# Kernel tuning notes

Hardware: AMD Instinct MI355X
Metric: run time of the kernel (lower is better)

The kernel has to match this reference:

```python
import jax, jax.numpy as jnp
import numpy as np

B, L, D, H = 2, 4096, 1024, 4
DV = D // H
NP = 5
MIN_PROB = 0.01
CHUNK = 32
RIN = D + H * NP * 4 + H * (NP * (NP - 1)) // 2  # 1144
RH = 2 * RIN


def dwconv_causal(x, w):
    # x: (B, L, C); w: (C, K) depthwise causal FIR
    K = w.shape[-1]
    xp = jnp.pad(x, ((0, 0), (K - 1, 0), (0, 0))).transpose(0, 2, 1)  # (B,C,L+K-1)
    y = jax.lax.conv_general_dilated(
        xp, w[:, None, :], window_strides=(1,), padding='VALID',
        feature_group_count=w.shape[0],
        dimension_numbers=('NCH', 'OIH', 'NCH'))
    return y.transpose(0, 2, 1)  # (B,L,C)


def l2norm(x):
    return x * jax.lax.rsqrt(jnp.sum(x * x, -1, keepdims=True) + 1e-12)


def delta_rule_chunkwise(q, k, v, beta, chunk=CHUNK):
    # q,k: (b,h,L,dk)  v: (b,h,L,dv)  beta: (b,h,L); L divisible by chunk
    b, h, Lq, dk = q.shape
    dv = v.shape[-1]
    n = Lq // chunk
    q = l2norm(q); k = l2norm(k)
    v = v * beta[..., None]
    kb = k * beta[..., None]
    r = lambda x: x.reshape(b, h, n, chunk, -1)
    q, k, v, kb = r(q), r(k), r(v), r(kb)
    tri = jnp.triu(jnp.ones((chunk, chunk), bool), 0)
    attn = jnp.where(tri, 0.0, -(kb @ jnp.swapaxes(k, -1, -2)))
    for i in range(1, chunk):  # in-chunk triangular-inverse recurrence
        upd = jnp.einsum('...k,...ki->...i', attn[..., i, :], attn[..., :, :i])
        attn = attn.at[..., i, :i].add(upd)
    attn = attn + jnp.eye(chunk, dtype=attn.dtype)
    u = attn @ v
    w = attn @ kb
    strict = jnp.triu(jnp.ones((chunk, chunk), bool), 1)

    def step(S, inp):
        qi, ki, ui, wi = inp
        la = jnp.where(strict, 0.0, qi @ jnp.swapaxes(ki, -1, -2))
        u_i = ui - wi @ S
        o_i = qi @ S + la @ u_i
        return S + jnp.swapaxes(ki, -1, -2) @ u_i, o_i

    mv = lambda x: jnp.moveaxis(x, 2, 0)
    S0 = jnp.zeros((b, h, dk, dv), q.dtype)
    S, o = jax.lax.scan(step, S0, (mv(q), mv(k), mv(u), mv(w)))
    return jnp.moveaxis(o, 0, 2).reshape(b, h, Lq, dv), S


def setup_inputs() -> dict:
    key = jax.random.key(0)
    ks = jax.random.split(key, 20)
    f = lambda k, shape, s=0.02: jax.random.normal(k, shape, jnp.float32) * s
    # FIR filters: identity tap (last) + small noise, matching learned-from-delta init
    def fir(k, ksz):
        w = np.zeros((D, ksz), np.float32)
        w[:, -1] = 1.0
        return jnp.asarray(w) + f(k, (D, ksz), 0.02)
    b2 = np.zeros((H, NP), np.float32)
    b2[:, -1] = 0.5
    b2[:, -2] = 0.5
    return {
        'hidden_states': jax.random.normal(ks[0], (B, L, D), jnp.float32),
        'Wq': f(ks[1], (D, D)), 'Wk': f(ks[2], (D, D)), 'Wv': f(ks[3], (D, D)),
        'wq_conv': f(ks[4], (D, 4), 0.2), 'wk_conv': f(ks[5], (D, 4), 0.2),
        'wv_conv': f(ks[6], (D, 4), 0.2),
        'Wb': f(ks[7], (H, D)),
        'fir_s_w': fir(ks[8], 3), 'fir_m_w': fir(ks[9], 7),
        'fir_l_w': fir(ks[10], 25), 'fir_id_w': fir(ks[11], 1),
        'W1': f(ks[12], (RH, RIN)), 'b1': jnp.zeros((RH,), jnp.float32),
        'W2': f(ks[13], (H * NP, RH)), 'b2': jnp.asarray(b2.reshape(-1)),
        'norm_w': jnp.ones((DV,), jnp.float32),
        'Wo': f(ks[14], (D, D)),
    }


def reference(hidden_states, Wq, Wk, Wv, wq_conv, wk_conv, wv_conv, Wb,
              fir_s_w, fir_m_w, fir_l_w, fir_id_w, W1, b1, W2, b2, norm_w, Wo):
    silu = jax.nn.silu
    q = silu(dwconv_causal(hidden_states @ Wq.T, wq_conv))
    k = silu(dwconv_causal(hidden_states @ Wk.T, wk_conv))
    v = silu(dwconv_causal(hidden_states @ Wv.T, wv_conv))
    beta = jax.nn.sigmoid(hidden_states @ Wb.T)  # (B,L,H)
    q4 = q.reshape(B, L, H, -1).transpose(0, 2, 1, 3)
    k4 = k.reshape(B, L, H, -1).transpose(0, 2, 1, 3)
    v4 = v.reshape(B, L, H, -1).transpose(0, 2, 1, 3)
    delta_out, _ = delta_rule_chunkwise(q4, k4, v4, beta.transpose(0, 2, 1))
    delta_out = delta_out.transpose(0, 2, 1, 3)  # (B,L,H,DV)
    fir = lambda w: dwconv_causal(v, w).reshape(B, L, H, DV)
    branches = [fir(fir_s_w), fir(fir_m_w), fir(fir_l_w), delta_out, fir(fir_id_w)]
    feats = []
    for x in branches:
        sm = jax.nn.softmax(x, -1)
        feats += [x.mean(-1), jnp.var(x, -1, ddof=1), jnp.max(x, -1),
                  -(sm * jnp.log(sm + 1e-8)).sum(-1)]
    cross = []
    for i in range(NP):
        for j in range(i + 1, NP):
            xi, xj = branches[i], branches[j]
            den = jnp.sqrt(jnp.sum(xi * xi, -1)) * jnp.sqrt(jnp.sum(xj * xj, -1)) + 1e-8
            cross.append(jnp.sum(xi * xj, -1) / den)
    router_in = jnp.concatenate([hidden_states] + feats + cross, axis=-1)  # (B,L,RIN)
    hrt = jax.nn.gelu(router_in @ W1.T + b1, approximate=False)
    logits = (hrt @ W2.T + b2).reshape(B, L, H, NP)
    p = jax.nn.softmax(logits, -1)
    p = p * (1.0 - NP * MIN_PROB) + MIN_PROB  # probability floor
    out = jnp.einsum('blhp,pblhd->blhd', p, jnp.stack(branches))
    out = out * jax.lax.rsqrt(jnp.mean(out * out, -1, keepdims=True) + 1e-5) * norm_w
    return out.reshape(B, L, H * DV) @ Wo.T
```

## Files before the change

### kernel.cpp

```cpp
#include <hip/hip_runtime.h>
#include <stdint.h>

typedef unsigned short u16t;
typedef u16t us4 __attribute__((ext_vector_type(4)));
typedef u16t us8 __attribute__((ext_vector_type(8)));
typedef __bf16 bf8v __attribute__((ext_vector_type(8)));
typedef float f4 __attribute__((ext_vector_type(4)));

#define MFMA(a, b, c) __builtin_amdgcn_mfma_f32_16x16x32_bf16((a), (b), (c), 0, 0, 0)
#define GLOAD_LDS16(g, l) __builtin_amdgcn_global_load_lds( \
    (const __attribute__((address_space(1))) void*)(g),     \
    (__attribute__((address_space(3))) void*)(l), 16, 0, 0)

__device__ __forceinline__ float bf2f(u16t u) {
  union { unsigned int i; float f; } c; c.i = ((unsigned int)u) << 16; return c.f;
}
__device__ __forceinline__ u16t f2bf(float f) {
  union { float f; unsigned int i; } c; c.f = f;
  return (u16t)((c.i + 0x7FFFu + ((c.i >> 16) & 1u)) >> 16);
}
__device__ __forceinline__ float wsum(float v) {
#pragma unroll
  for (int o = 32; o > 0; o >>= 1) v += __shfl_xor(v, o);
  return v;
}
__device__ __forceinline__ float wmax(float v) {
#pragma unroll
  for (int o = 32; o > 0; o >>= 1) v = fmaxf(v, __shfl_xor(v, o));
  return v;
}

__global__ __launch_bounds__(256) void pack_all(const float* __restrict__ hid,
    const float* __restrict__ Wq, const float* __restrict__ Wk, const float* __restrict__ Wv,
    u16t* __restrict__ hidb, u16t* __restrict__ wqb, u16t* __restrict__ wkb,
    u16t* __restrict__ wvb) {
  const int g = blockIdx.x * 256 + threadIdx.x;
  const float* src; u16t* dst; int off;
  if (g < 2097152) { src = hid; dst = hidb; off = g; }
  else if (g < 2359296) { src = Wq; dst = wqb; off = g - 2097152; }
  else if (g < 2621440) { src = Wk; dst = wkb; off = g - 2359296; }
  else { src = Wv; dst = wvb; off = g - 2621440; }
  f4 v = *(const f4*)&src[(size_t)off * 4];
  us4 o;
#pragma unroll
  for (int e = 0; e < 4; ++e) o[e] = f2bf(v[e]);
  *(us4*)&dst[(size_t)off * 4] = o;
}

__global__ __launch_bounds__(256) void pack_bf16(const float* __restrict__ src,
    u16t* __restrict__ dst, int n4) {
  const int i = blockIdx.x * 256 + threadIdx.x;
  if (i >= n4) return;
  f4 v = *(const f4*)&src[(size_t)i * 4];
  us4 o;
#pragma unroll
  for (int e = 0; e < 4; ++e) o[e] = f2bf(v[e]);
  *(us4*)&dst[(size_t)i * 4] = o;
}

template <bool CF32, int EPI>
__device__ __forceinline__ void gemm_body(const u16t* __restrict__ A,
    const u16t* __restrict__ Bt, void* __restrict__ Cv, const float* __restrict__ bias,
    int K, int lda, int ldb, int ldc, int m0, int n0) {
  __shared__ u16t As[128][32];
  __shared__ u16t Bs[128][32];
  const int tid = threadIdx.x;
  const int wv = tid >> 6, l = tid & 63;
  const int wr = wv >> 1, wc = wv & 1;
  const int lr = l & 15, kg8 = (l >> 4) * 8, rg4 = (l >> 4) * 4;
  const f4 zf = {0.f, 0.f, 0.f, 0.f};
  f4 acc[4][4];
#pragma unroll
  for (int i = 0; i < 4; ++i)
#pragma unroll
    for (int j = 0; j < 4; ++j) acc[i][j] = zf;

  const u16t* ga = A + (size_t)(m0 + wv * 32 + (l >> 2)) * lda + (l & 3) * 8;
  const u16t* gb = Bt + (size_t)(n0 + wv * 32 + (l >> 2)) * ldb + (l & 3) * 8;
  u16t* la0 = &As[wv * 32][0];
  u16t* la1 = &As[wv * 32 + 16][0];
  u16t* lb0 = &Bs[wv * 32][0];
  u16t* lb1 = &Bs[wv * 32 + 16][0];

  for (int kt = 0; kt < K; kt += 32) {
    GLOAD_LDS16(ga + kt, la0);
    GLOAD_LDS16(ga + (size_t)16 * lda + kt, la1);
    GLOAD_LDS16(gb + kt, lb0);
    GLOAD_LDS16(gb + (size_t)16 * ldb + kt, lb1);
    __syncthreads();
    bf8v af[4], bg[4];
#pragma unroll
    for (int f = 0; f < 4; ++f) af[f] = *(const bf8v*)&As[wr * 64 + f * 16 + lr][kg8];
#pragma unroll
    for (int f = 0; f < 4; ++f) bg[f] = *(const bf8v*)&Bs[wc * 64 + f * 16 + lr][kg8];
#pragma unroll
    for (int i = 0; i < 4; ++i)
#pragma unroll
      for (int j = 0; j < 4; ++j) acc[i][j] = MFMA(af[i], bg[j], acc[i][j]);
    __syncthreads();
  }
#pragma unroll
  for (int i = 0; i < 4; ++i) {
    const int rb = m0 + wr * 64 + i * 16 + rg4;
#pragma unroll
    for (int j = 0; j < 4; ++j) {
      const int cb = n0 + wc * 64 + j * 16 + lr;
#pragma unroll
      for (int r = 0; r < 4; ++r) {
        float x = acc[i][j][r];
        if (EPI == 1) {
          float xx = x + ((cb < 2288) ? bias[cb] : 0.f);
          x = 0.5f * xx * (1.f + erff(xx * 0.70710678118f));
        }
        if (CF32)
          ((float*)Cv)[(size_t)(rb + r) * ldc + cb] = x;
        else
          ((u16t*)Cv)[(size_t)(rb + r) * ldc + cb] = f2bf(x);
      }
    }
  }
}

template <bool CF32, int EPI>
__global__ __launch_bounds__(256) void gemm_bt(const u16t* __restrict__ Av,
    const u16t* __restrict__ Btv, void* __restrict__ Cv, const float* __restrict__ bias,
    int K, int lda, int ldb, int ldc) {
  gemm_body<CF32, EPI>(Av, Btv, Cv, bias, K, lda, ldb, ldc,
                       blockIdx.y * 128, blockIdx.x * 128);
}

__global__ __launch_bounds__(256) void gemm_qkv3(const u16t* __restrict__ A,
    const u16t* __restrict__ B0, const u16t* __restrict__ B1,
    const u16t* __restrict__ B2, u16t* __restrict__ C0, u16t* __restrict__ C1,
    u16t* __restrict__ C2v) {
  const int z = blockIdx.z;
  const u16t* Bt = (z == 0) ? B0 : ((z == 1) ? B1 : B2);
  u16t* C = (z == 0) ? C0 : ((z == 1) ? C1 : C2v);
  gemm_body<false, 0>(A, Bt, C, nullptr, 1024, 1024, 1024, 1024,
                      blockIdx.y * 128, blockIdx.x * 128);
}
// ... 14 lines not shown
  for (int i = 0; i < 67; ++i) {
    int ls = l0 - 3 + i;
    sm[i][tid] = (ls >= 0) ? in_[((size_t)b * 4096 + ls) * 1024 + c] : (u16t)0;
  }
  __syncthreads();
  f4 w4 = *(const f4*)&w_[c * 4];
  float x0 = bf2f(sm[0][tid]), x1 = bf2f(sm[1][tid]), x2 = bf2f(sm[2][tid]);
  for (int ll = 0; ll < 64; ++ll) {
    float x3 = bf2f(sm[ll + 3][tid]);
    float y = x0 * w4[0] + x1 * w4[1] + x2 * w4[2] + x3 * w4[3];
    y = y / (1.f + expf(-y));
    out_[((size_t)b * 4096 + l0 + ll) * 1024 + c] = f2bf(y);
    x0 = x1; x1 = x2; x2 = x3;
  }
}

__global__ __launch_bounds__(256) void prep_kernel(u16t* __restrict__ qc, u16t* __restrict__ kc,
    const u16t* __restrict__ vc, const float* __restrict__ hid, const float* __restrict__ Wb,
    u16t* __restrict__ kbeta, u16t* __restrict__ vbeta) {
  const int m = blockIdx.x, tid = threadIdx.x;
  const int h = tid >> 6, l = tid & 63;
  float bacc = 0.f;
#pragma unroll
  for (int it = 0; it < 4; ++it) {
    int kk = l * 4 + it * 256;
    f4 hv = *(const f4*)&hid[(size_t)m * 1024 + kk];
    f4 wv4 = *(const f4*)&Wb[(size_t)h * 1024 + kk];
#pragma unroll
    for (int e = 0; e < 4; ++e) bacc += hv[e] * wv4[e];
  }
  const float bet = 1.f / (1.f + expf(-wsum(bacc)));
  const size_t base = (size_t)m * 1024 + h * 256 + l * 4;
  us4 q4 = *(const us4*)&qc[base];
  float qf[4]; float ss = 0.f;
#pragma unroll
  for (int e = 0; e < 4; ++e) { qf[e] = bf2f(q4[e]); ss += qf[e] * qf[e]; }
  float qsc = rsqrtf(wsum(ss) + 1e-12f);
  us4 qo;
#pragma unroll
  for (int e = 0; e < 4; ++e) qo[e] = f2bf(qf[e] * qsc);
  *(us4*)&qc[base] = qo;
  us4 k4 = *(const us4*)&kc[base];
  float kf[4]; ss = 0.f;
#pragma unroll
  for (int e = 0; e < 4; ++e) { kf[e] = bf2f(k4[e]); ss += kf[e] * kf[e]; }
  float ksc = rsqrtf(wsum(ss) + 1e-12f);
  us4 ko, kbo;
#pragma unroll
  for (int e = 0; e < 4; ++e) {
    float kn = kf[e] * ksc;
    ko[e] = f2bf(kn);
    kbo[e] = f2bf(kn * bet);
  }
  *(us4*)&kc[base] = ko;
  *(us4*)&kbeta[base] = kbo;
  us4 v4 = *(const us4*)&vc[base];
  us4 vo;
#pragma unroll
  for (int e = 0; e < 4; ++e) vo[e] = f2bf(bf2f(v4[e]) * bet);
  *(us4*)&vbeta[base] = vo;
}

__global__ __launch_bounds__(256) void chunk_uw(const u16t* __restrict__ kn,
    const u16t* __restrict__ kbeta, const u16t* __restrict__ vbeta,
    u16t* __restrict__ ug, u16t* __restrict__ wg) {
  const int tid = threadIdx.x;
  const int bh = blockIdx.x >> 7, ci = blockIdx.x & 127;
  const int b = bh >> 2, h = bh & 3;
  const int l0 = ci * 32;
  __shared__ u16t kns[32][264], kbs[32][264], vbs[32][264];
  __shared__ float attn_s[32][33];
  const int sr = tid >> 5, sd8 = (tid & 31) * 8;
  const size_t rowbase = (size_t)b * 4096 * 1024 + (size_t)h * 256;
#pragma unroll
  for (int i = 0; i < 4; ++i) {
    int r = i * 8 + sr;
    size_t g = rowbase + (size_t)(l0 + r) * 1024 + sd8;
    *(us8*)&kns[r][sd8] = *(const us8*)&kn[g];
    *(us8*)&kbs[r][sd8] = *(const us8*)&kbeta[g];
    *(us8*)&vbs[r][sd8] = *(const us8*)&vbeta[g];
  }
  __syncthreads();
  {
    const int i = tid >> 3, j4 = (tid & 7) * 4;
    float d0 = 0.f, d1 = 0.f, d2 = 0.f, d3 = 0.f;
    for (int d8 = 0; d8 < 256; d8 += 8) {
      us8 kb8 = *(const us8*)&kbs[i][d8];
      us8 n0v = *(const us8*)&kns[j4][d8];
      us8 n1v = *(const us8*)&kns[j4 + 1][d8];
      us8 n2v = *(const us8*)&kns[j4 + 2][d8];
      us8 n3v = *(const us8*)&kns[j4 + 3][d8];
#pragma unroll
      for (int e = 0; e < 8; ++e) {
        float kv = bf2f(kb8[e]);
        d0 += kv * bf2f(n0v[e]); d1 += kv * bf2f(n1v[e]);
        d2 += kv * bf2f(n2v[e]); d3 += kv * bf2f(n3v[e]);
      }
    }
    attn_s[i][j4]     = (j4     < i) ? -d0 : 0.f;
    attn_s[i][j4 + 1] = (j4 + 1 < i) ? -d1 : 0.f;
    attn_s[i][j4 + 2] = (j4 + 2 < i) ? -d2 : 0.f;
    attn_s[i][j4 + 3] = (j4 + 3 < i) ? -d3 : 0.f;
  }
  __syncthreads();
  if (tid < 32) {
    const int j = tid;
    for (int i = 1; i < 32; ++i) {
      float aij = attn_s[i][j];
      float upd = 0.f;
#pragma unroll 1
      for (int k = 1; k < 31; ++k) {
        float aik = __shfl(aij, k);
        float akj = (k > j && k < i) ? attn_s[k][j] : 0.f;
        upd += aik * akj;
      }
      if (j < i) attn_s[i][j] = aij + upd;
    }
    attn_s[j][j] = 1.f;
  }
  __syncthreads();
  {
    const int r = tid >> 3, cg = (tid & 7) * 32;
    float ua[32], wa[32];
#pragma unroll
    for (int e = 0; e < 32; ++e) { ua[e] = 0.f; wa[e] = 0.f; }
    for (int j = 0; j < 32; ++j) {
      float a = attn_s[r][j];
#pragma unroll
      for (int e0 = 0; e0 < 32; e0 += 8) {
        us8 v8 = *(const us8*)&vbs[j][cg + e0];
        us8 k8 = *(const us8*)&kbs[j][cg + e0];
#pragma unroll
        for (int e = 0; e < 8; ++e) {
          ua[e0 + e] += a * bf2f(v8[e]);
          wa[e0 + e] += a * bf2f(k8[e]);
        }
      }
    }
    const size_t ob = ((size_t)bh * 4096 + l0 + r) * 256 + cg;
#pragma unroll
    for (int e0 = 0; e0 < 32; e0 += 8) {
      us8 pu, pw;
#pragma unroll
      for (int e = 0; e < 8; ++e) { pu[e] = f2bf(ua[e0 + e]); pw[e] = f2bf(wa[e0 + e]); }
      *(us8*)&ug[ob + e0] = pu;
      *(us8*)&wg[ob + e0] = pw;
    }
  }
}

__global__ __launch_bounds__(256, 1) void delta_scan(const u16t* __restrict__ qn,
    const u16t* __restrict__ kn, const u16t* __restrict__ ug, const u16t* __restrict__ wg,
    u16t* __restrict__ dout, const u16t* __restrict__ vc, const float* __restrict__ w25g,
    u16t* __restrict__ fl, const float* __restrict__ W1, u16t* __restrict__ W1p,
    const float* __restrict__ Wo, u16t* __restrict__ wob) {
  const int blk = blockIdx.x;
  const int tid = threadIdx.x;
  if (blk < 32) {
    const int bh = blk >> 2, vbidx = blk & 3;
    const int b = bh >> 2, h = bh & 3;
    const int c0 = vbidx * 64;
    const int wv = tid >> 6, l = tid & 63;
    const int lr = l & 15, kg8 = (l >> 4) * 8, rg4 = (l >> 4) * 4;

    __shared__ u16t qs[32][264], ks2[32][264], wss[32][264];
    __shared__ u16t kts[256][40];
    __shared__ u16t sbf[64][264];
    __shared__ u16t las[32][40];
    __shared__ u16t uts[64][40];

    {
      u16t* sp = &sbf[0][0];
      for (int i = tid; i < 64 * 264; i += 256) sp[i] = 0;
    }
    const f4 zf = {0.f, 0.f, 0.f, 0.f};
    f4 sacc[16];
#pragma unroll
    for (int d = 0; d < 16; ++d) sacc[d] = zf;
    __syncthreads();

    const u16t* qb = qn + (size_t)b * 4096 * 1024 + (size_t)h * 256;
    const u16t* knb = kn + (size_t)b * 4096 * 1024 + (size_t)h * 256;
    const u16t* ub = ug + (size_t)bh * 4096 * 256;
    const u16t* wb = wg + (size_t)bh * 4096 * 256;
    const int sr = tid >> 5, sd8 = (tid & 31) * 8;

    us8 pq[4], pk[4], pw[4];
    us4 pu0, pu1;
#pragma unroll
    for (int i = 0; i < 4; ++i) {
      const int r = i * 8 + sr;
      pq[i] = *(const us8*)(qb + (size_t)r * 1024 + sd8);
      pk[i] = *(const us8*)(knb + (size_t)r * 1024 + sd8);
      pw[i] = *(const us8*)(wb + (size_t)r * 256 + sd8);
    }
    pu0 = *(const us4*)(ub + (size_t)lr * 256 + c0 + wv * 16 + rg4);
    pu1 = *(const us4*)(ub + (size_t)(16 + lr) * 256 + c0 + wv * 16 + rg4);

    for (int ci = 0; ci < 128; ++ci) {
      const int l0 = ci * 32;
#pragma unroll
      for (int i = 0; i < 4; ++i) {
        const int r = i * 8 + sr;
        *(us8*)&qs[r][sd8] = pq[i];
        *(us8*)&ks2[r][sd8] = pk[i];
        *(us8*)&wss[r][sd8] = pw[i];
      }
      const us4 u0 = pu0, u1 = pu1;
      __syncthreads();
      if (ci < 127) {
        const int l1 = l0 + 32;
#pragma unroll
        for (int i = 0; i < 4; ++i) {
          const int r = i * 8 + sr;
          pq[i] = *(const us8*)(qb + (size_t)(l1 + r) * 1024 + sd8);
          pk[i] = *(const us8*)(knb + (size_t)(l1 + r) * 1024 + sd8);
          pw[i] = *(const us8*)(wb + (size_t)(l1 + r) * 256 + sd8);
        }
        pu0 = *(const us4*)(ub + (size_t)(l1 + lr) * 256 + c0 + wv * 16 + rg4);
        pu1 = *(const us4*)(ub + (size_t)(l1 + 16 + lr) * 256 + c0 + wv * 16 + rg4);
      }
      {
        const int dk = tid;
        const int swz = ((dk >> 3) & 3) << 3;
#pragma unroll
        for (int r = 0; r < 32; r += 2) {
          unsigned int lo = ks2[r][dk], hi = ks2[r + 1][dk];
          *(unsigned int*)&kts[dk][r ^ swz] = lo | (hi << 16);
        }
      }
      {
        const int rq = wv >> 1, rk = wv & 1;
        f4 t4 = zf;
#pragma unroll
        for (int ks = 0; ks < 8; ++ks) {
          bf8v a = *(const bf8v*)&qs[rq * 16 + lr][ks * 32 + kg8];
          bf8v bb = *(const bf8v*)&ks2[rk * 16 + lr][ks * 32 + kg8];
          t4 = MFMA(a, bb, t4);
// ... 24 lines not shown
        for (int rt = 0; rt < 2; ++rt) {
          f4 mm = rt ? m1 : m0;
          const us4 uu = rt ? u1 : u0;
          const int r = rt * 16 + lr;
#pragma unroll
          for (int rr = 0; rr < 4; ++rr)
            uts[wv * 16 + rg4 + rr][r] = f2bf(bf2f(uu[rr]) - mm[rr]);
        }
      }
      __syncthreads();
      {
        bf8v a2 = *(const bf8v*)&uts[wv * 16 + lr][kg8];
        {
          bf8v lb0 = *(const bf8v*)&las[lr][kg8];
          bf8v lb1 = *(const bf8v*)&las[16 + lr][kg8];
          o0 = MFMA(a2, lb0, o0);
          o1 = MFMA(a2, lb1, o1);
        }
#pragma unroll
        for (int rt = 0; rt < 2; ++rt) {
          f4 oo = rt ? o1 : o0;
          const int r = rt * 16 + lr;
          us4 st;
#pragma unroll
          for (int rr = 0; rr < 4; ++rr) st[rr] = f2bf(oo[rr]);
          *(us4*)(dout + ((size_t)(b * 4096 + l0 + r) * 4 + h) * 256 + c0 + wv * 16 + rg4) = st;
        }
#pragma unroll
        for (int d = 0; d < 16; ++d) {
          const int swzd = ((2 * d + (lr >> 3)) & 3) << 3;
          bf8v bb = *(const bf8v*)&kts[d * 16 + lr][kg8 ^ swzd];
          sacc[d] = MFMA(a2, bb, sacc[d]);
        }
#pragma unroll
        for (int d = 0; d < 16; ++d) {
#pragma unroll
          for (int rr = 0; rr < 4; ++rr)
            sbf[wv * 16 + rg4 + rr][d * 16 + lr] = f2bf(sacc[d][rr]);
        }
      }
      __syncthreads();
    }
    return;
  }
  if (blk < 544) {
    const int fb = blk - 32;
    const int l0 = (fb & 63) * 64;
    const int by = fb >> 6;
    const int b = by >> 2, cb = by & 3;
    const int c = cb * 256 + tid;
    __shared__ u16t sm[88][256];
    for (int i = 0; i < 88; ++i) {
      int ls = l0 - 24 + i;
      sm[i][tid] = (ls >= 0) ? vc[((size_t)b * 4096 + ls) * 1024 + c] : (u16t)0;
    }
    __syncthreads();
    float w25[25];
#pragma unroll
    for (int j = 0; j < 25; ++j) w25[j] = w25g[c * 25 + j];
    float x[25];
#pragma unroll
    for (int j = 0; j < 25; ++j) x[j] = bf2f(sm[j][tid]);
    for (int ll = 0; ll < 64; ++ll) {
      float yl = 0.f;
#pragma unroll
      for (int j = 0; j < 25; ++j) yl += x[j] * w25[j];
      fl[((size_t)b * 4096 + l0 + ll) * 1024 + c] = f2bf(yl);
      if (ll < 63) {
#pragma unroll
        for (int j = 0; j < 24; ++j) x[j] = x[j + 1];
        x[24] = bf2f(sm[ll + 25][tid]);
      }
    }
    return;
  }
  if (blk < 672) {
    for (size_t idx = (size_t)(blk - 544) * 256 + tid; idx < (size_t)2304 * 1152;
         idx += (size_t)128 * 256) {
      int n = (int)(idx / 1152), k = (int)(idx % 1152);
      W1p[idx] = (n < 2288 && k < 1144) ? f2bf(W1[(size_t)n * 1144 + k]) : (u16t)0;
    }
    return;
  }
  for (size_t i = (size_t)(blk - 672) * 256 + tid; i < 262144; i += (size_t)64 * 256) {
    f4 v = *(const f4*)&Wo[i * 4];
    us4 o;
#pragma unroll
    for (int e = 0; e < 4; ++e) o[e] = f2bf(v[e]);
    *(us4*)&wob[i * 4] = o;
  }
}

__device__ __forceinline__ void fir_otf(const u16t* __restrict__ vc,
    const float* __restrict__ w3g, const float* __restrict__ w7g,
    const float* __restrict__ w1g, int b, int lseq, int c0,
    float ys[4], float ym[4], float yi[4]) {
  float xs[7][4];
#pragma unroll
  for (int j = 0; j < 7; ++j) {
    int ls = lseq - 6 + j;
    if (ls >= 0) {
      us4 v = *(const us4*)&vc[((size_t)b * 4096 + ls) * 1024 + c0];
#pragma unroll
      for (int e = 0; e < 4; ++e) xs[j][e] = bf2f(v[e]);
    } else {
#pragma unroll
      for (int e = 0; e < 4; ++e) xs[j][e] = 0.f;
    }
  }
#pragma unroll
  for (int e = 0; e < 4; ++e) {
    const int c = c0 + e;
    ys[e] = xs[4][e] * w3g[c * 3] + xs[5][e] * w3g[c * 3 + 1] + xs[6][e] * w3g[c * 3 + 2];
    float m_ = 0.f;
#pragma unroll
    for (int j = 0; j < 7; ++j) m_ += xs[j][e] * w7g[c * 7 + j];
    ym[e] = m_;
    yi[e] = xs[6][e] * w1g[c];
  }
}

__global__ __launch_bounds__(256) void features_kernel(const float* __restrict__ hid,
    const u16t* __restrict__ vc, const float* __restrict__ w3g, const float* __restrict__ w7g,
    const float* __restrict__ w1g, const u16t* __restrict__ fl, const u16t* __restrict__ dlt,
    u16t* __restrict__ router) {
  const int m = blockIdx.x, tid = threadIdx.x;
  const int h = tid >> 6, l = tid & 63;
  const int b = m >> 12, lseq = m & 4095;
  const int c0 = h * 256 + l * 4;
  const size_t base = (size_t)m * 1024 + c0;
  float x[5][4];
  fir_otf(vc, w3g, w7g, w1g, b, lseq, c0, x[0], x[1], x[4]);
  {
    us4 v2 = *(const us4*)&fl[base];
    us4 v3 = *(const us4*)&dlt[base];
#pragma unroll
    for (int e = 0; e < 4; ++e) { x[2][e] = bf2f(v2[e]); x[3][e] = bf2f(v3[e]); }
  }
  float s1[5], s2[5], mx[5];
#pragma unroll
  for (int br = 0; br < 5; ++br) {
    float a = 0.f, bq = 0.f, m_ = -1e30f;
#pragma unroll
    for (int e = 0; e < 4; ++e) {
      a += x[br][e]; bq += x[br][e] * x[br][e]; m_ = fmaxf(m_, x[br][e]);
    }
    s1[br] = wsum(a); s2[br] = wsum(bq); mx[br] = wmax(m_);
  }
  float ent[5];
#pragma unroll
  for (int br = 0; br < 5; ++br) {
    float e_ = 0.f;
#pragma unroll
    for (int e = 0; e < 4; ++e) e_ += expf(x[br][e] - mx[br]);
    float es = wsum(e_);
    float hn = 0.f;
#pragma unroll
    for (int e = 0; e < 4; ++e) {
      float pv = expf(x[br][e] - mx[br]) / es;
      hn += pv * logf(pv + 1e-8f);
    }
    ent[br] = -wsum(hn);
  }
  float dt[10];
  {
    int pi = 0;
#pragma unroll
    for (int i = 0; i < 5; ++i)
#pragma unroll
      for (int j = i + 1; j < 5; ++j) {
        float d = 0.f;
#pragma unroll
        for (int e = 0; e < 4; ++e) d += x[i][e] * x[j][e];
        dt[pi] = wsum(d);
        ++pi;
      }
  }
  if (l == 0) {
    u16t* rp = router + (size_t)m * 1152 + 1024;
#pragma unroll
    for (int br = 0; br < 5; ++br) {
      float mean = s1[br] * (1.f / 256.f);
      float var = (s2[br] - s1[br] * s1[br] * (1.f / 256.f)) * (1.f / 255.f);
      rp[br * 16 + 0 + h] = f2bf(mean);
      rp[br * 16 + 4 + h] = f2bf(var);
      rp[br * 16 + 8 + h] = f2bf(mx[br]);
      rp[br * 16 + 12 + h] = f2bf(ent[br]);
    }
    int pi = 0;
#pragma unroll
    for (int i = 0; i < 5; ++i)
#pragma unroll
      for (int j = i + 1; j < 5; ++j) {
        float den = sqrtf(s2[i]) * sqrtf(s2[j]) + 1e-8f;
        rp[80 + pi * 4 + h] = f2bf(dt[pi] / den);
        ++pi;
      }
  }
  {
    f4 hv = *(const f4*)&hid[(size_t)m * 1024 + tid * 4];
    us4 hv4;
#pragma unroll
    for (int e = 0; e < 4; ++e) hv4[e] = f2bf(hv[e]);
    *(us4*)&router[(size_t)m * 1152 + tid * 4] = hv4;
  }
  if (tid < 8) router[(size_t)m * 1152 + 1144 + tid] = 0;
}

__global__ __launch_bounds__(256) void w2_softmax(const u16t* __restrict__ hrt,
    const float* __restrict__ W2, const float* __restrict__ b2, float* __restrict__ pout) {
  const int m = blockIdx.x, tid = threadIdx.x;
  const int h = tid >> 6, l = tid & 63;
  float acc[5];
#pragma unroll
  for (int n = 0; n < 5; ++n) acc[n] = 0.f;
  for (int kk = l * 4; kk < 2288; kk += 256) {
    us4 hv = *(const us4*)&hrt[(size_t)m * 2304 + kk];
    float hf[4];
#pragma unroll
    for (int e = 0; e < 4; ++e) hf[e] = bf2f(hv[e]);
#pragma unroll
    for (int n = 0; n < 5; ++n) {
      f4 wv4 = *(const f4*)&W2[(size_t)(h * 5 + n) * 2288 + kk];
#pragma unroll
      for (int e = 0; e < 4; ++e) acc[n] += hf[e] * wv4[e];
    }
  }
#pragma unroll
  for (int n = 0; n < 5; ++n) acc[n] = wsum(acc[n]);
  if (l == 0) {
    float lg[5];
#pragma unroll
    for (int n = 0; n < 5; ++n) lg[n] = acc[n] + b2[h * 5 + n];
    float mxv = lg[0];
#pragma unroll
    for (int n = 1; n < 5; ++n) mxv = fmaxf(mxv, lg[n]);
    float es = 0.f, ev[5];
#pragma unroll
    for (int n = 0; n < 5; ++n) { ev[n] = expf(lg[n] - mxv); es += ev[n]; }
#pragma unroll
    for (int n = 0; n < 5; ++n)
      pout[(size_t)m * 20 + h * 5 + n] = (ev[n] / es) * 0.95f + 0.01f;
  }
}

__global__ __launch_bounds__(256) void mix_kernel(const u16t* __restrict__ vc,
    const float* __restrict__ w3g, const float* __restrict__ w7g,
    const float* __restrict__ w1g, const u16t* __restrict__ fl,
    const u16t* __restrict__ dlt, const float* __restrict__ pbuf,
    const float* __restrict__ normw, u16t* __restrict__ mixed) {
  const int m = blockIdx.x, tid = threadIdx.x;
  const int h = tid >> 6, l = tid & 63;
  const int b = m >> 12, lseq = m & 4095;
  const int c0 = h * 256 + l * 4;
  const size_t base = (size_t)m * 1024 + c0;
  float x[5][4];
  fir_otf(vc, w3g, w7g, w1g, b, lseq, c0, x[0], x[1], x[4]);
  {
    us4 v2 = *(const us4*)&fl[base];
    us4 v3 = *(const us4*)&dlt[base];
#pragma unroll
    for (int e = 0; e < 4; ++e) { x[2][e] = bf2f(v2[e]); x[3][e] = bf2f(v3[e]); }
  }
  float p5[5];
#pragma unroll
  for (int n = 0; n < 5; ++n) p5[n] = pbuf[(size_t)m * 20 + h * 5 + n];
  float o[4] = {0.f, 0.f, 0.f, 0.f};
#pragma unroll
  for (int br = 0; br < 5; ++br)
#pragma unroll
    for (int e = 0; e < 4; ++e) o[e] += p5[br] * x[br][e];
  float ss = 0.f;
#pragma unroll
  for (int e = 0; e < 4; ++e) ss += o[e] * o[e];
  ss = wsum(ss);
  float sc = rsqrtf(ss * (1.f / 256.f) + 1e-5f);
  f4 nw = *(const f4*)&normw[l * 4];
  us4 ov;
#pragma unroll
  for (int e = 0; e < 4; ++e) ov[e] = f2bf(o[e] * sc * nw[e]);
  *(us4*)&mixed[base] = ov;
}

extern "C" void kernel_launch(void* const* d_in, const int* in_sizes, int n_in,
                              void* d_out, int out_size, void* d_ws, size_t ws_size,
                              hipStream_t stream) {
  (void)in_sizes; (void)n_in; (void)out_size; (void)ws_size;
  const float* hid = (const float*)d_in[0];
  const float* Wq = (const float*)d_in[1];
  const float* Wk = (const float*)d_in[2];
  const float* Wv = (const float*)d_in[3];
  const float* wqc = (const float*)d_in[4];
  const float* wkc = (const float*)d_in[5];
  const float* wvc = (const float*)d_in[6];
  const float* Wb = (const float*)d_in[7];
  const float* fsw = (const float*)d_in[8];
  const float* fmw = (const float*)d_in[9];
  const float* flw = (const float*)d_in[10];
  const float* fiw = (const float*)d_in[11];
  const float* W1 = (const float*)d_in[12];
  const float* b1 = (const float*)d_in[13];
  const float* W2 = (const float*)d_in[14];
  const float* b2 = (const float*)d_in[15];
  const float* nwt = (const float*)d_in[16];
  const float* Wo = (const float*)d_in[17];
  float* out = (float*)d_out;

  char* wsp = (char*)d_ws;
  const size_t S = (size_t)2 * 4096 * 1024 * 2;
  u16t* ql = (u16t*)(wsp + 0 * S);
  u16t* kl = (u16t*)(wsp + 1 * S);
  u16t* vl = (u16t*)(wsp + 2 * S);
  u16t* qc = (u16t*)(wsp + 3 * S);
  u16t* kc = (u16t*)(wsp + 4 * S);
  u16t* vc = (u16t*)(wsp + 5 * S);
  u16t* ubuf = (u16t*)(wsp + 6 * S);
  u16t* wbuf = (u16t*)(wsp + 7 * S);
  char* p = wsp + 8 * S;
  u16t* router = (u16t*)p; p += (size_t)8192 * 1152 * 2;
  u16t* hrt = (u16t*)p;    p += (size_t)8192 * 2304 * 2;
  u16t* w1p = (u16t*)p;    p += (size_t)2304 * 1152 * 2;
  float* pbuf = (float*)p; p += (size_t)8192 * 20 * 4;
  u16t* wob = (u16t*)p;    p += (size_t)1024 * 1024 * 2;
  u16t* hidb = qc;
  u16t* wqb = kc;
  u16t* wkb = kc + 1048576;
  u16t* wvb = kc + 2097152;
  u16t* kbeta = ql;
  u16t* vbeta = kl;
  u16t* dlt = kl;
  u16t* f_l = vl;
  u16t* mixed = wbuf;

  dim3 blk(256);
  pack_all<<<dim3(11264), blk, 0, stream>>>(hid, Wq, Wk, Wv, hidb, wqb, wkb, wvb);
  gemm_qkv3<<<dim3(8, 64, 3), blk, 0, stream>>>(hidb, wqb, wkb, wvb, ql, kl, vl);
  conv4_silu<<<dim3(64, 8, 3), blk, 0, stream>>>(ql, kl, vl, wqc, wkc, wvc, qc, kc, vc);
  prep_kernel<<<dim3(8192), blk, 0, stream>>>(qc, kc, vc, hid, Wb, kbeta, vbeta);
  chunk_uw<<<dim3(1024), blk, 0, stream>>>(kc, kbeta, vbeta, ubuf, wbuf);
  delta_scan<<<dim3(736), blk, 0, stream>>>(qc, kc, ubuf, wbuf, dlt, vc, flw, f_l, W1, w1p, Wo, wob);
  features_kernel<<<dim3(8192), blk, 0, stream>>>(hid, vc, fsw, fmw, fiw, f_l, dlt, router);
  gemm_bt<false, 1><<<dim3(18, 64), blk, 0, stream>>>(router, w1p, hrt, b1, 1152, 1152, 1152, 2304);
  w2_softmax<<<dim3(8192), blk, 0, stream>>>(hrt, W2, b2, pbuf);
  mix_kernel<<<dim3(8192), blk, 0, stream>>>(vc, fsw, fmw, fiw, f_l, dlt, pbuf, nwt, mixed);
  gemm_bt<true, 0><<<dim3(8, 64), blk, 0, stream>>>(mixed, wob, out, nullptr, 1024, 1024, 1024, 1024);
}
```

Before: 1.056 ms.

## Overlap non-delta router features with scan, fuse W2 softmax into mix, MFMA attn

Result: slower. 1.424 ms (+34.8%).

```diff
diff --git a/kernel.cpp b/kernel.cpp
--- a/kernel.cpp
+++ b/kernel.cpp
@@ -45,17 +45,6 @@
 #pragma unroll
   for (int e = 0; e < 4; ++e) o[e] = f2bf(v[e]);
   *(us4*)&dst[(size_t)off * 4] = o;
-}
-
-__global__ __launch_bounds__(256) void pack_bf16(const float* __restrict__ src,
-    u16t* __restrict__ dst, int n4) {
-  const int i = blockIdx.x * 256 + threadIdx.x;
-  if (i >= n4) return;
-  f4 v = *(const f4*)&src[(size_t)i * 4];
-  us4 o;
-#pragma unroll
-  for (int e = 0; e < 4; ++e) o[e] = f2bf(v[e]);
-  *(us4*)&dst[(size_t)i * 4] = o;
 }
 
 template <bool CF32, int EPI>
@@ -236,25 +225,22 @@
   }
   __syncthreads();
   {
-    const int i = tid >> 3, j4 = (tid & 7) * 4;
-    float d0 = 0.f, d1 = 0.f, d2 = 0.f, d3 = 0.f;
-    for (int d8 = 0; d8 < 256; d8 += 8) {
-      us8 kb8 = *(const us8*)&kbs[i][d8];
-      us8 n0v = *(const us8*)&kns[j4][d8];
-      us8 n1v = *(const us8*)&kns[j4 + 1][d8];
-      us8 n2v = *(const us8*)&kns[j4 + 2][d8];
-      us8 n3v = *(const us8*)&kns[j4 + 3][d8];
-#pragma unroll
-      for (int e = 0; e < 8; ++e) {
-        float kv = bf2f(kb8[e]);
-        d0 += kv * bf2f(n0v[e]); d1 += kv * bf2f(n1v[e]);
-        d2 += kv * bf2f(n2v[e]); d3 += kv * bf2f(n3v[e]);
-      }
-    }
-    attn_s[i][j4]     = (j4     < i) ? -d0 : 0.f;
-    attn_s[i][j4 + 1] = (j4 + 1 < i) ? -d1 : 0.f;
-    attn_s[i][j4 + 2] = (j4 + 2 < i) ? -d2 : 0.f;
-    attn_s[i][j4 + 3] = (j4 + 3 < i) ? -d3 : 0.f;
+    const int wv = tid >> 6, l = tid & 63;
+    const int lr = l & 15, kg8 = (l >> 4) * 8, rg4 = (l >> 4) * 4;
+    const int rq = wv >> 1, rk = wv & 1;
+    f4 t4 = {0.f, 0.f, 0.f, 0.f};
+#pragma unroll
+    for (int ks = 0; ks < 8; ++ks) {
+      bf8v a = *(const bf8v*)&kbs[rq * 16 + lr][ks * 32 + kg8];
+      bf8v bb = *(const bf8v*)&kns[rk * 16 + lr][ks * 32 + kg8];
+      t4 = MFMA(a, bb, t4);
+    }
+    const int colj = rk * 16 + lr;
+#pragma unroll
+    for (int rr = 0; rr < 4; ++rr) {
+      const int rowr = rq * 16 + rg4 + rr;
+      attn_s[rowr][colj] = (colj < rowr) ? -t4[rr] : 0.f;
+    }
   }
   __syncthreads();
   if (tid < 32) {
@@ -307,7 +293,9 @@
     const u16t* __restrict__ kn, const u16t* __restrict__ ug, const u16t* __restrict__ wg,
     u16t* __restrict__ dout, const u16t* __restrict__ vc, const float* __restrict__ w25g,
     u16t* __restrict__ fl, const float* __restrict__ W1, u16t* __restrict__ W1p,
-    const float* __restrict__ Wo, u16t* __restrict__ wob) {
+    const float* __restrict__ Wo, u16t* __restrict__ wob, const float* __restrict__ hid,
+    const float* __restrict__ w3g, const float* __restrict__ w7g,
+    const float* __restrict__ w1g, u16t* __restrict__ router, float* __restrict__ s2buf) {
   const int blk = blockIdx.x;
   const int tid = threadIdx.x;
   if (blk < 32) {
@@ -498,12 +486,116 @@
     }
     return;
   }
-  for (size_t i = (size_t)(blk - 672) * 256 + tid; i < 262144; i += (size_t)64 * 256) {
-    f4 v = *(const f4*)&Wo[i * 4];
-    us4 o;
-#pragma unroll
-    for (int e = 0; e < 4; ++e) o[e] = f2bf(v[e]);
-    *(us4*)&wob[i * 4] = o;
+  if (blk < 736) {
+    for (size_t i = (size_t)(blk - 672) * 256 + tid; i < 262144; i += (size_t)64 * 256) {
+      f4 v = *(const f4*)&Wo[i * 4];
+      us4 o;
+#pragma unroll
+      for (int e = 0; e < 4; ++e) o[e] = f2bf(v[e]);
+      *(us4*)&wob[i * 4] = o;
+    }
+    return;
+  }
+  {
+    const int m = blk - 736;
+    const int h = tid >> 6, l = tid & 63;
+    const int b = m >> 12, lseq = m & 4095;
+    const int c0 = h * 256 + l * 4;
+    float xb[4][4];
+    {
+      float win[7][4];
+      float x25[4] = {0.f, 0.f, 0.f, 0.f};
+#pragma unroll
+      for (int j = 0; j < 25; ++j) {
+        float xv[4];
+        int ls = lseq - 24 + j;
+        if (ls >= 0) {
+          us4 v = *(const us4*)&vc[((size_t)b * 4096 + ls) * 1024 + c0];
+#pragma unroll
+          for (int e = 0; e < 4; ++e) xv[e] = bf2f(v[e]);
+        } else {
+#pragma unroll
+          for (int e = 0; e < 4; ++e) xv[e] = 0.f;
+        }
+#pragma unroll
+        for (int e = 0; e < 4; ++e) x25[e] += xv[e] * w25g[(c0 + e) * 25 + j];
+        if (j >= 18) {
+#pragma unroll
+          for (int e = 0; e < 4; ++e) win[j - 18][e] = xv[e];
+        }
+      }
+#pragma unroll
+      for (int e = 0; e < 4; ++e) {
+        const int c = c0 + e;
+        xb[0][e] = win[4][e] * w3g[c * 3] + win[5][e] * w3g[c * 3 + 1] +
+                   win[6][e] * w3g[c * 3 + 2];
+        float m_ = 0.f;
+#pragma unroll
+        for (int j = 0; j < 7; ++j) m_ += win[j][e] * w7g[c * 7 + j];
+        xb[1][e] = m_;
+        xb[2][e] = x25[e];
+        xb[3][e] = win[6][e] * w1g[c];
+      }
+    }
+    float s1[4], s2[4], mx[4], ent[4];
+#pragma unroll
+    for (int bi = 0; bi < 4; ++bi) {
+      float a = 0.f, bq = 0.f, m_ = -1e30f;
+#pragma unroll
+      for (int e = 0; e < 4; ++e) {
+        a += xb[bi][e]; bq += xb[bi][e] * xb[bi][e]; m_ = fmaxf(m_, xb[bi][e]);
+      }
+      s1[bi] = wsum(a); s2[bi] = wsum(bq); mx[bi] = wmax(m_);
+      float ee[4], e_ = 0.f;
+#pragma unroll
+      for (int e = 0; e < 4; ++e) { ee[e] = expf(xb[bi][e] - mx[bi]); e_ += ee[e]; }
+      float es = wsum(e_);
+      float hn = 0.f;
+#pragma unroll
+      for (int e = 0; e < 4; ++e) {
+        float pv = ee[e] / es;
+        hn += pv * logf(pv + 1e-8f);
+      }
+      ent[bi] = -wsum(hn);
+    }
+    const int pidx[6] = {0, 1, 3, 4, 6, 8};
+    const int pa_[6] = {0, 0, 0, 1, 1, 2};
+    const int pb_[6] = {1, 2, 3, 2, 3, 3};
+    float dts[6];
+#pragma unroll
+    for (int pi = 0; pi < 6; ++pi) {
+      float d = 0.f;
+#pragma unroll
+      for (int e = 0; e < 4; ++e) d += xb[pa_[pi]][e] * xb[pb_[pi]][e];
+      dts[pi] = wsum(d);
+    }
+    if (l == 0) {
+      u16t* rp = router + (size_t)m * 1152 + 1024;
+      const int slot[4] = {0, 1, 2, 4};
+#pragma unroll
+      for (int bi = 0; bi < 4; ++bi) {
+        float mean = s1[bi] * (1.f / 256.f);
+        float var = (s2[bi] - s1[bi] * s1[bi] * (1.f / 256.f)) * (1.f / 255.f);
+        rp[slot[bi] * 16 + 0 + h] = f2bf(mean);
+        rp[slot[bi] * 16 + 4 + h] = f2bf(var);
+        rp[slot[bi] * 16 + 8 + h] = f2bf(mx[bi]);
+        rp[slot[bi] * 16 + 12 + h] = f2bf(ent[bi]);
+        s2buf[((size_t)m * 4 + h) * 4 + bi] = s2[bi];
+      }
+#pragma unroll
+      for (int pi = 0; pi < 6; ++pi) {
+        float den = sqrtf(s2[pa_[pi]]) * sqrtf(s2[pb_[pi]]) + 1e-8f;
+        rp[80 + pidx[pi] * 4 + h] = f2bf(dts[pi] / den);
+      }
+    }
+    {
+      f4 hv = *(const f4*)&hid[(size_t)m * 1024 + tid * 4];
+      us4 hv4;
+#pragma unroll
+      for (int e = 0; e < 4; ++e) hv4[e] = f2bf(hv[e]);
+      *(us4*)&router[(size_t)m * 1152 + tid * 4] = hv4;
+    }
+    if (tid < 8) router[(size_t)m * 1152 + 1144 + tid] = 0;
   }
 }
 
@@ -536,12 +628,100 @@
   }
 }
 
-__global__ __launch_bounds__(256) void features_kernel(const float* __restrict__ hid,
-    const u16t* __restrict__ vc, const float* __restrict__ w3g, const float* __restrict__ w7g,
-    const float* __restrict__ w1g, const u16t* __restrict__ fl, const u16t* __restrict__ dlt,
+__global__ __launch_bounds__(256) void features_post(const u16t* __restrict__ vc,
+    const float* __restrict__ w3g, const float* __restrict__ w7g,
+    const float* __restrict__ w1g, const u16t* __restrict__ fl,
+    const u16t* __restrict__ dlt, const float* __restrict__ s2buf,
     u16t* __restrict__ router) {
   const int m = blockIdx.x, tid = threadIdx.x;
   const int h = tid >> 6, l = tid & 63;
+  const int b = m >> 12, lseq = m & 4095;
+  const int c0 = h * 256 + l * 4;
+  const size_t base = (size_t)m * 1024 + c0;
+  float x0[4], x1[4], x4[4], x2[4], x3[4];
+  fir_otf(vc, w3g, w7g, w1g, b, lseq, c0, x0, x1, x4);
+  {
+    us4 v2 = *(const us4*)&fl[base];
+    us4 v3 = *(const us4*)&dlt[base];
+#pragma unroll
+    for (int e = 0; e < 4; ++e) { x2[e] = bf2f(v2[e]); x3[e] = bf2f(v3[e]); }
+  }
+  float a = 0.f, bq = 0.f, m_ = -1e30f;
+#pragma unroll
+  for (int e = 0; e < 4; ++e) { a += x3[e]; bq += x3[e] * x3[e]; m_ = fmaxf(m_, x3[e]); }
+  float s1_3 = wsum(a), s2_3 = wsum(bq), mx3 = wmax(m_);
+  float ee[4], e_ = 0.f;
+#pragma unroll
+  for (int e = 0; e < 4; ++e) { ee[e] = expf(x3[e] - mx3); e_ += ee[e]; }
+  float es = wsum(e_);
+  float hn = 0.f;
+#pragma unroll
+  for (int e = 0; e < 4; ++e) {
+    float pv = ee[e] / es;
+    hn += pv * logf(pv + 1e-8f);
+  }
+  float ent3 = -wsum(hn);
+  float d03 = 0.f, d13 = 0.f, d23 = 0.f, d34 = 0.f;
+#pragma unroll
+  for (int e = 0; e < 4; ++e) {
+    d03 += x0[e] * x3[e]; d13 += x1[e] * x3[e];
+    d23 += x2[e] * x3[e]; d34 += x3[e] * x4[e];
+  }
+  d03 = wsum(d03); d13 = wsum(d13); d23 = wsum(d23); d34 = wsum(d34);
+  if (l == 0) {
+    u16t* rp = router + (size_t)m * 1152 + 1024;
+    float mean = s1_3 * (1.f / 256.f);
+    float var = (s2_3 - s1_3 * s1_3 * (1.f / 256.f)) * (1.f / 255.f);
+    rp[3 * 16 + 0 + h] = f2bf(mean);
+    rp[3 * 16 + 4 + h] = f2bf(var);
+    rp[3 * 16 + 8 + h] = f2bf(mx3);
+    rp[3 * 16 + 12 + h] = f2bf(ent3);
+    const float* sb = &s2buf[((size_t)m * 4 + h) * 4];
+    float r3 = sqrtf(s2_3);
+    rp[80 + 2 * 4 + h] = f2bf(d03 / (sqrtf(sb[0]) * r3 + 1e-8f));
+    rp[80 + 5 * 4 + h] = f2bf(d13 / (sqrtf(sb[1]) * r3 + 1e-8f));
+    rp[80 + 7 * 4 + h] = f2bf(d23 / (sqrtf(sb[2]) * r3 + 1e-8f));
+    rp[80 + 9 * 4 + h] = f2bf(d34 / (r3 * sqrtf(sb[3]) + 1e-8f));
+  }
+}
+
+__global__ __launch_bounds__(256) void route_mix(const u16t* __restrict__ hrt,
+    const float* __restrict__ W2, const float* __restrict__ b2,
+    const u16t* __restrict__ vc, const float* __restrict__ w3g,
+    const float* __restrict__ w7g, const float* __restrict__ w1g,
+    const u16t* __restrict__ fl, const u16t* __restrict__ dlt,
+    const float* __restrict__ normw, u16t* __restrict__ mixed) {
+  const int m = blockIdx.x, tid = threadIdx.x;
+  const int h = tid >> 6, l = tid & 63;
+  float acc[5];
+#pragma unroll
+  for (int n = 0; n < 5; ++n) acc[n] = 0.f;
+  for (int kk = l * 4; kk < 2288; kk += 256) {
+    us4 hv = *(const us4*)&hrt[(size_t)m * 2304 + kk];
+    float hf[4];
+#pragma unroll
+    for (int e = 0; e < 4; ++e) hf[e] = bf2f(hv[e]);
+#pragma unroll
+    for (int n = 0; n < 5; ++n) {
+      f4 wv4 = *(const f4*)&W2[(size_t)(h * 5 + n) * 2288 + kk];
+#pragma unroll
+      for (int e = 0; e < 4; ++e) acc[n] += hf[e] * wv4[e];
+    }
+  }
+  float p5[5];
+  {
+    float lg[5];
+#pragma unroll
+    for (int n = 0; n < 5; ++n) lg[n] = wsum(acc[n]) + b2[h * 5 + n];
+    float mxv = lg[0];
+#pragma unroll
+    for (int n = 1; n < 5; ++n) mxv = fmaxf(mxv, lg[n]);
+    float es = 0.f, ev[5];
+#pragma unroll
+    for (int n = 0; n < 5; ++n) { ev[n] = expf(lg[n] - mxv); es += ev[n]; }
+#pragma unroll
+    for (int n = 0; n < 5; ++n) p5[n] = (ev[n] / es) * 0.95f + 0.01f;
+  }
   const int b = m >> 12, lseq = m & 4095;
   const int c0 = h * 256 + l * 4;
   const size_t base = (size_t)m * 1024 + c0;
@@ -553,134 +733,6 @@
 #pragma unroll
     for (int e = 0; e < 4; ++e) { x[2][e] = bf2f(v2[e]); x[3][e] = bf2f(v3[e]); }
   }
-  float s1[5], s2[5], mx[5];
-#pragma unroll
-  for (int br = 0; br < 5; ++br) {
-    float a = 0.f, bq = 0.f, m_ = -1e30f;
-#pragma unroll
-    for (int e = 0; e < 4; ++e) {
-      a += x[br][e]; bq += x[br][e] * x[br][e]; m_ = fmaxf(m_, x[br][e]);
-    }
-    s1[br] = wsum(a); s2[br] = wsum(bq); mx[br] = wmax(m_);
-  }
-  float ent[5];
-#pragma unroll
-  for (int br = 0; br < 5; ++br) {
-    float e_ = 0.f;
-#pragma unroll
-    for (int e = 0; e < 4; ++e) e_ += expf(x[br][e] - mx[br]);
-    float es = wsum(e_);
-    float hn = 0.f;
-#pragma unroll
-    for (int e = 0; e < 4; ++e) {
-      float pv = expf(x[br][e] - mx[br]) / es;
-      hn += pv * logf(pv + 1e-8f);
-    }
-    ent[br] = -wsum(hn);
-  }
-  float dt[10];
-  {
-    int pi = 0;
-#pragma unroll
-    for (int i = 0; i < 5; ++i)
-#pragma unroll
-      for (int j = i + 1; j < 5; ++j) {
-        float d = 0.f;
-#pragma unroll
-        for (int e = 0; e < 4; ++e) d += x[i][e] * x[j][e];
-        dt[pi] = wsum(d);
-        ++pi;
-      }
-  }
-  if (l == 0) {
-    u16t* rp = router + (size_t)m * 1152 + 1024;
-#pragma unroll
-    for (int br = 0; br < 5; ++br) {
-      float mean = s1[br] * (1.f / 256.f);
-      float var = (s2[br] - s1[br] * s1[br] * (1.f / 256.f)) * (1.f / 255.f);
-      rp[br * 16 + 0 + h] = f2bf(mean);
-      rp[br * 16 + 4 + h] = f2bf(var);
-      rp[br * 16 + 8 + h] = f2bf(mx[br]);
-      rp[br * 16 + 12 + h] = f2bf(ent[br]);
-    }
-    int pi = 0;
-#pragma unroll
-    for (int i = 0; i < 5; ++i)
-#pragma unroll
-      for (int j = i + 1; j < 5; ++j) {
-        float den = sqrtf(s2[i]) * sqrtf(s2[j]) + 1e-8f;
-        rp[80 + pi * 4 + h] = f2bf(dt[pi] / den);
-        ++pi;
-      }
-  }
-  {
-    f4 hv = *(const f4*)&hid[(size_t)m * 1024 + tid * 4];
-    us4 hv4;
-#pragma unroll
-    for (int e = 0; e < 4; ++e) hv4[e] = f2bf(hv[e]);
-    *(us4*)&router[(size_t)m * 1152 + tid * 4] = hv4;
-  }
-  if (tid < 8) router[(size_t)m * 1152 + 1144 + tid] = 0;
-}
-
-__global__ __launch_bounds__(256) void w2_softmax(const u16t* __restrict__ hrt,
-    const float* __restrict__ W2, const float* __restrict__ b2, float* __restrict__ pout) {
-  const int m = blockIdx.x, tid = threadIdx.x;
-  const int h = tid >> 6, l = tid & 63;
-  float acc[5];
-#pragma unroll
-  for (int n = 0; n < 5; ++n) acc[n] = 0.f;
-  for (int kk = l * 4; kk < 2288; kk += 256) {
-    us4 hv = *(const us4*)&hrt[(size_t)m * 2304 + kk];
-    float hf[4];
-#pragma unroll
-    for (int e = 0; e < 4; ++e) hf[e] = bf2f(hv[e]);
-#pragma unroll
-    for (int n = 0; n < 5; ++n) {
-      f4 wv4 = *(const f4*)&W2[(size_t)(h * 5 + n) * 2288 + kk];
-#pragma unroll
-      for (int e = 0; e < 4; ++e) acc[n] += hf[e] * wv4[e];
-    }
-  }
-#pragma unroll
-  for (int n = 0; n < 5; ++n) acc[n] = wsum(acc[n]);
-  if (l == 0) {
-    float lg[5];
-#pragma unroll
-    for (int n = 0; n < 5; ++n) lg[n] = acc[n] + b2[h * 5 + n];
-    float mxv = lg[0];
-#pragma unroll
-    for (int n = 1; n < 5; ++n) mxv = fmaxf(mxv, lg[n]);
-    float es = 0.f, ev[5];
-#pragma unroll
-    for (int n = 0; n < 5; ++n) { ev[n] = expf(lg[n] - mxv); es += ev[n]; }
-#pragma unroll
-    for (int n = 0; n < 5; ++n)
-      pout[(size_t)m * 20 + h * 5 + n] = (ev[n] / es) * 0.95f + 0.01f;
-  }
-}
-
-__global__ __launch_bounds__(256) void mix_kernel(const u16t* __restrict__ vc,
-    const float* __restrict__ w3g, const float* __restrict__ w7g,
-    const float* __restrict__ w1g, const u16t* __restrict__ fl,
-    const u16t* __restrict__ dlt, const float* __restrict__ pbuf,
-    const float* __restrict__ normw, u16t* __restrict__ mixed) {
-  const int m = blockIdx.x, tid = threadIdx.x;
-  const int h = tid >> 6, l = tid & 63;
-  const int b = m >> 12, lseq = m & 4095;
-  const int c0 = h * 256 + l * 4;
-  const size_t base = (size_t)m * 1024 + c0;
-  float x[5][4];
-  fir_otf(vc, w3g, w7g, w1g, b, lseq, c0, x[0], x[1], x[4]);
-  {
-    us4 v2 = *(const us4*)&fl[base];
-    us4 v3 = *(const us4*)&dlt[base];
-#pragma unroll
-    for (int e = 0; e < 4; ++e) { x[2][e] = bf2f(v2[e]); x[3][e] = bf2f(v3[e]); }
-  }
-  float p5[5];
-#pragma unroll
-  for (int n = 0; n < 5; ++n) p5[n] = pbuf[(size_t)m * 20 + h * 5 + n];
   float o[4] = {0.f, 0.f, 0.f, 0.f};
 #pragma unroll
   for (int br = 0; br < 5; ++br)
@@ -736,8 +788,8 @@
   u16t* router = (u16t*)p; p += (size_t)8192 * 1152 * 2;
   u16t* hrt = (u16t*)p;    p += (size_t)8192 * 2304 * 2;
   u16t* w1p = (u16t*)p;    p += (size_t)2304 * 1152 * 2;
-  float* pbuf = (float*)p; p += (size_t)8192 * 20 * 4;
   u16t* wob = (u16t*)p;    p += (size_t)1024 * 1024 * 2;
+  float* s2buf = (float*)p; p += (size_t)8192 * 4 * 4 * 4;
   u16t* hidb = qc;
   u16t* wqb = kc;
   u16t* wkb = kc + 1048576;
@@ -754,10 +806,11 @@
   conv4_silu<<<dim3(64, 8, 3), blk, 0, stream>>>(ql, kl, vl, wqc, wkc, wvc, qc, kc, vc);
   prep_kernel<<<dim3(8192), blk, 0, stream>>>(qc, kc, vc, hid, Wb, kbeta, vbeta);
   chunk_uw<<<dim3(1024), blk, 0, stream>>>(kc, kbeta, vbeta, ubuf, wbuf);
-  delta_scan<<<dim3(736), blk, 0, stream>>>(qc, kc, ubuf, wbuf, dlt, vc, flw, f_l, W1, w1p, Wo, wob);
-  features_kernel<<<dim3(8192), blk, 0, stream>>>(hid, vc, fsw, fmw, fiw, f_l, dlt, router);
+  delta_scan<<<dim3(8928), blk, 0, stream>>>(qc, kc, ubuf, wbuf, dlt, vc, flw, f_l,
+                                             W1, w1p, Wo, wob, hid, fsw, fmw, fiw,
+                                             router, s2buf);
+  features_post<<<dim3(8192), blk, 0, stream>>>(vc, fsw, fmw, fiw, f_l, dlt, s2buf, router);
   gemm_bt<false, 1><<<dim3(18, 64), blk, 0, stream>>>(router, w1p, hrt, b1, 1152, 1152, 1152, 2304);
-  w2_softmax<<<dim3(8192), blk, 0, stream>>>(hrt, W2, b2, pbuf);
-  mix_kernel<<<dim3(8192), blk, 0, stream>>>(vc, fsw, fmw, fiw, f_l, dlt, pbuf, nwt, mixed);
+  route_mix<<<dim3(8192), blk, 0, stream>>>(hrt, W2, b2, vc, fsw, fmw, fiw, f_l, dlt, nwt, mixed);
   gemm_bt<true, 0><<<dim3(8, 64), blk, 0, stream>>>(mixed, wob, out, nullptr, 1024, 1024, 1024, 1024);
 }
```

## Fuse router softmax into mix kernel and use MFMA for chunk attention

Applied to the files above, without the earlier changes.

Result: no change. 1.039 ms (-1.6%).

```diff
diff --git a/kernel.cpp b/kernel.cpp
--- a/kernel.cpp
+++ b/kernel.cpp
@@ -45,17 +45,6 @@
 #pragma unroll
   for (int e = 0; e < 4; ++e) o[e] = f2bf(v[e]);
   *(us4*)&dst[(size_t)off * 4] = o;
-}
-
-__global__ __launch_bounds__(256) void pack_bf16(const float* __restrict__ src,
-    u16t* __restrict__ dst, int n4) {
-  const int i = blockIdx.x * 256 + threadIdx.x;
-  if (i >= n4) return;
-  f4 v = *(const f4*)&src[(size_t)i * 4];
-  us4 o;
-#pragma unroll
-  for (int e = 0; e < 4; ++e) o[e] = f2bf(v[e]);
-  *(us4*)&dst[(size_t)i * 4] = o;
 }
 
 template <bool CF32, int EPI>
@@ -236,25 +225,22 @@
   }
   __syncthreads();
   {
-    const int i = tid >> 3, j4 = (tid & 7) * 4;
-    float d0 = 0.f, d1 = 0.f, d2 = 0.f, d3 = 0.f;
-    for (int d8 = 0; d8 < 256; d8 += 8) {
-      us8 kb8 = *(const us8*)&kbs[i][d8];
-      us8 n0v = *(const us8*)&kns[j4][d8];
-      us8 n1v = *(const us8*)&kns[j4 + 1][d8];
-      us8 n2v = *(const us8*)&kns[j4 + 2][d8];
-      us8 n3v = *(const us8*)&kns[j4 + 3][d8];
-#pragma unroll
-      for (int e = 0; e < 8; ++e) {
-        float kv = bf2f(kb8[e]);
-        d0 += kv * bf2f(n0v[e]); d1 += kv * bf2f(n1v[e]);
-        d2 += kv * bf2f(n2v[e]); d3 += kv * bf2f(n3v[e]);
-      }
-    }
-    attn_s[i][j4]     = (j4     < i) ? -d0 : 0.f;
-    attn_s[i][j4 + 1] = (j4 + 1 < i) ? -d1 : 0.f;
-    attn_s[i][j4 + 2] = (j4 + 2 < i) ? -d2 : 0.f;
-    attn_s[i][j4 + 3] = (j4 + 3 < i) ? -d3 : 0.f;
+    const int wv = tid >> 6, l = tid & 63;
+    const int lr = l & 15, kg8 = (l >> 4) * 8, rg4 = (l >> 4) * 4;
+    const int rq = wv >> 1, rk = wv & 1;
+    f4 t4 = {0.f, 0.f, 0.f, 0.f};
+#pragma unroll
+    for (int ks = 0; ks < 8; ++ks) {
+      bf8v a = *(const bf8v*)&kbs[rq * 16 + lr][ks * 32 + kg8];
+      bf8v bb = *(const bf8v*)&kns[rk * 16 + lr][ks * 32 + kg8];
+      t4 = MFMA(a, bb, t4);
+    }
+    const int colj = rk * 16 + lr;
+#pragma unroll
+    for (int rr = 0; rr < 4; ++rr) {
+      const int rowr = rq * 16 + rg4 + rr;
+      attn_s[rowr][colj] = (colj < rowr) ? -t4[rr] : 0.f;
+    }
   }
   __syncthreads();
   if (tid < 32) {
@@ -623,8 +609,12 @@
   if (tid < 8) router[(size_t)m * 1152 + 1144 + tid] = 0;
 }
 
-__global__ __launch_bounds__(256) void w2_softmax(const u16t* __restrict__ hrt,
-    const float* __restrict__ W2, const float* __restrict__ b2, float* __restrict__ pout) {
+__global__ __launch_bounds__(256) void route_mix(const u16t* __restrict__ hrt,
+    const float* __restrict__ W2, const float* __restrict__ b2,
+    const u16t* __restrict__ vc, const float* __restrict__ w3g,
+    const float* __restrict__ w7g, const float* __restrict__ w1g,
+    const u16t* __restrict__ fl, const u16t* __restrict__ dlt,
+    const float* __restrict__ normw, u16t* __restrict__ mixed) {
   const int m = blockIdx.x, tid = threadIdx.x;
   const int h = tid >> 6, l = tid & 63;
   float acc[5];
@@ -642,12 +632,11 @@
       for (int e = 0; e < 4; ++e) acc[n] += hf[e] * wv4[e];
     }
   }
-#pragma unroll
-  for (int n = 0; n < 5; ++n) acc[n] = wsum(acc[n]);
-  if (l == 0) {
+  float p5[5];
+  {
     float lg[5];
 #pragma unroll
-    for (int n = 0; n < 5; ++n) lg[n] = acc[n] + b2[h * 5 + n];
+    for (int n = 0; n < 5; ++n) lg[n] = wsum(acc[n]) + b2[h * 5 + n];
     float mxv = lg[0];
 #pragma unroll
     for (int n = 1; n < 5; ++n) mxv = fmaxf(mxv, lg[n]);
@@ -655,18 +644,8 @@
 #pragma unroll
     for (int n = 0; n < 5; ++n) { ev[n] = expf(lg[n] - mxv); es += ev[n]; }
 #pragma unroll
-    for (int n = 0; n < 5; ++n)
-      pout[(size_t)m * 20 + h * 5 + n] = (ev[n] / es) * 0.95f + 0.01f;
-  }
-}
-
-__global__ __launch_bounds__(256) void mix_kernel(const u16t* __restrict__ vc,
-    const float* __restrict__ w3g, const float* __restrict__ w7g,
-    const float* __restrict__ w1g, const u16t* __restrict__ fl,
-    const u16t* __restrict__ dlt, const float* __restrict__ pbuf,
-    const float* __restrict__ normw, u16t* __restrict__ mixed) {
-  const int m = blockIdx.x, tid = threadIdx.x;
-  const int h = tid >> 6, l = tid & 63;
+    for (int n = 0; n < 5; ++n) p5[n] = (ev[n] / es) * 0.95f + 0.01f;
+  }
   const int b = m >> 12, lseq = m & 4095;
   const int c0 = h * 256 + l * 4;
   const size_t base = (size_t)m * 1024 + c0;
@@ -678,9 +657,6 @@
 #pragma unroll
     for (int e = 0; e < 4; ++e) { x[2][e] = bf2f(v2[e]); x[3][e] = bf2f(v3[e]); }
   }
-  float p5[5];
-#pragma unroll
-  for (int n = 0; n < 5; ++n) p5[n] = pbuf[(size_t)m * 20 + h * 5 + n];
   float o[4] = {0.f, 0.f, 0.f, 0.f};
 #pragma unroll
   for (int br = 0; br < 5; ++br)
@@ -736,7 +712,6 @@
   u16t* router = (u16t*)p; p += (size_t)8192 * 1152 * 2;
   u16t* hrt = (u16t*)p;    p += (size_t)8192 * 2304 * 2;
   u16t* w1p = (u16t*)p;    p += (size_t)2304 * 1152 * 2;
-  float* pbuf = (float*)p; p += (size_t)8192 * 20 * 4;
   u16t* wob = (u16t*)p;    p += (size_t)1024 * 1024 * 2;
   u16t* hidb = qc;
   u16t* wqb = kc;
@@ -754,10 +729,10 @@
   conv4_silu<<<dim3(64, 8, 3), blk, 0, stream>>>(ql, kl, vl, wqc, wkc, wvc, qc, kc, vc);
   prep_kernel<<<dim3(8192), blk, 0, stream>>>(qc, kc, vc, hid, Wb, kbeta, vbeta);
   chunk_uw<<<dim3(1024), blk, 0, stream>>>(kc, kbeta, vbeta, ubuf, wbuf);
-  delta_scan<<<dim3(736), blk, 0, stream>>>(qc, kc, ubuf, wbuf, dlt, vc, flw, f_l, W1, w1p, Wo, wob);
+  delta_scan<<<dim3(736), blk, 0, stream>>>(qc, kc, ubuf, wbuf, dlt, vc, flw, f_l,
+                                            W1, w1p, Wo, wob);
   features_kernel<<<dim3(8192), blk, 0, stream>>>(hid, vc, fsw, fmw, fiw, f_l, dlt, router);
   gemm_bt<false, 1><<<dim3(18, 64), blk, 0, stream>>>(router, w1p, hrt, b1, 1152, 1152, 1152, 2304);
-  w2_softmax<<<dim3(8192), blk, 0, stream>>>(hrt, W2, b2, pbuf);
-  mix_kernel<<<dim3(8192), blk, 0, stream>>>(vc, fsw, fmw, fiw, f_l, dlt, pbuf, nwt, mixed);
+  route_mix<<<dim3(8192), blk, 0, stream>>>(hrt, W2, b2, vc, fsw, fmw, fiw, f_l, dlt, nwt, mixed);
   gemm_bt<true, 0><<<dim3(8, 64), blk, 0, stream>>>(mixed, wob, out, nullptr, 1024, 1024, 1024, 1024);
 }
```
